# Performance work log

Hardware: AMD Instinct MI355X
Metric: run time of the kernel (lower is better)

The kernel has to match this reference:

```python
import jax, jax.numpy as jnp
import numpy as np

L, H, P = 16384, 1024, 512
DT_MIN, DT_MAX = 1e-3, 1e-1
STEP_RESCALE = 1.0


def setup_inputs() -> dict:
    key = jax.random.key(0)
    ks = jax.random.split(key, 7)
    input_sequence = jax.random.normal(ks[0], (L, H), jnp.float32)
    # eigenvalues with negative real part (left half plane), HiPPO-like imag parts
    Lambda_re = -(jax.random.uniform(ks[1], (P,), jnp.float32) * 0.9 + 0.1)
    Lambda_im = jnp.pi * jnp.arange(P, dtype=jnp.float32)
    B = jax.random.normal(ks[2], (P, H, 2), jnp.float32) / jnp.sqrt(2.0 * H)   # real/imag of B_tilde (P,H)
    C = jax.random.normal(ks[3], (H, P, 2), jnp.float32) / jnp.sqrt(2.0 * P)   # real/imag of C_tilde (H,P)
    D = jax.random.normal(ks[4], (H,), jnp.float32)
    u01 = jax.random.uniform(ks[5], (P, 1), jnp.float32)
    log_step = jnp.log(DT_MIN) + u01 * (jnp.log(DT_MAX) - jnp.log(DT_MIN))     # (P,1)
    return dict(input_sequence=input_sequence, Lambda_re=Lambda_re, Lambda_im=Lambda_im,
                B=B, C=C, D=D, log_step=log_step)


def _binop(q_i, q_j):
    # diagonal linear recurrence composition: (A, b) pairs
    A_i, b_i = q_i
    A_j, b_j = q_j
    return A_j * A_i, A_j * b_i + b_j


def reference(input_sequence, Lambda_re, Lambda_im, B, C, D, log_step):
    Lambda = Lambda_re + 1j * Lambda_im                        # (P,) complex64
    B_tilde = B[..., 0] + 1j * B[..., 1]                       # (P,H)
    C_tilde = C[..., 0] + 1j * C[..., 1]                       # (H,P)
    step = STEP_RESCALE * jnp.exp(log_step[:, 0])              # (P,)
    # ZOH discretization
    Lambda_bar = jnp.exp(Lambda * step)                        # (P,)
    B_bar = ((Lambda_bar - 1.0) / Lambda)[:, None] * B_tilde   # (P,H)
    # Bu_elements: (L,P) complex
    Bu = input_sequence.astype(B_bar.dtype) @ B_bar.T
    Lambda_elems = jnp.broadcast_to(Lambda_bar, Bu.shape)      # (L,P)
    # parallel associative scan over the diagonal recurrence x_t = Lambda_bar*x_{t-1} + Bu_t
    _, xs = jax.lax.associative_scan(_binop, (Lambda_elems, Bu))
    ys = 2.0 * (xs @ C_tilde.T).real                           # conj_sym => factor 2, (L,H)
    return ys + D * input_sequence
```

## Files before the change

kernel.cpp:

```cpp
#include <hip/hip_runtime.h>
#include <math.h>

#define L_SEQ 16384
#define H_DIM 1024
#define P_DIM 512
#define N2P   1024
#define KDIM  1024
#define NKT   16
#define CHUNK 64
#define NCHUNK 256

typedef __attribute__((ext_vector_type(8))) short short8;
typedef __attribute__((ext_vector_type(4))) float f32x4;
typedef __attribute__((address_space(3))) const char* lds3_t;

__device__ __forceinline__ unsigned short f2bf(float f){
    unsigned int u = __float_as_uint(f);
    u = (u + 0x7FFFu + ((u >> 16) & 1u)) >> 16;
    return (unsigned short)u;
}
__device__ __forceinline__ float bf2f(unsigned int lo16){
    return __uint_as_float(lo16 << 16);
}

__global__ void k_prep_lambda(const float* __restrict__ lre, const float* __restrict__ lim,
                              const float* __restrict__ lstep,
                              float* __restrict__ lam, float* __restrict__ coef,
                              float* __restrict__ lpow, float* __restrict__ wtab)
{
    int p = threadIdx.x;
    double step = exp((double)lstep[p]);
    double dr = (double)lre[p], di = (double)lim[p];
    double ar = dr*step, ai = di*step;
    double er = exp(ar);
    double lbr = er*cos(ai), lbi = er*sin(ai);
    lam[2*p] = (float)lbr; lam[2*p+1] = (float)lbi;
    double nr = lbr - 1.0, ni = lbi;
    double d2 = dr*dr + di*di;
    coef[2*p]   = (float)((nr*dr + ni*di)/d2);
    coef[2*p+1] = (float)((ni*dr - nr*di)/d2);
    double pwr = 1.0, pwi = 0.0;
    for (int tt = 63; tt >= 0; --tt){
        wtab[((size_t)tt*P_DIM + p)*2]     = (float)pwr;
        wtab[((size_t)tt*P_DIM + p)*2 + 1] = (float)pwi;
        double t2 = pwr*lbr - pwi*lbi;
        pwi = pwr*lbi + pwi*lbr;
        pwr = t2;
    }
    double xr = lbr, xi = lbi;
    #pragma unroll
    for (int s=0;s<6;s++){ double t = xr*xr - xi*xi; xi = 2.0*xr*xi; xr = t; }
    lpow[2*p] = (float)xr; lpow[2*p+1] = (float)xi;
}

__global__ __launch_bounds__(256)
void k_prep_bc(const float* __restrict__ B, const float* __restrict__ C,
               const float* __restrict__ coef,
               unsigned short* __restrict__ BB, unsigned short* __restrict__ CC)
{
    int bid = blockIdx.x;
    if (bid < 2048){
        int i = bid*256 + threadIdx.x;
        int p = i >> 10, h = i & 1023;
        float br = B[2*i], bi = B[2*i+1];
        float cr = coef[2*p], ci = coef[2*p+1];
        BB[(size_t)(2*p)*H_DIM + h]   = f2bf(cr*br - ci*bi);
        BB[(size_t)(2*p+1)*H_DIM + h] = f2bf(cr*bi + ci*br);
    } else {
        int i = (bid-2048)*256 + threadIdx.x;
        int h = i >> 9, p = i & 511;
        float cr = C[2*i], ci = C[2*i+1];
        CC[(size_t)h*N2P + 2*p]     = f2bf(2.f*cr);
        CC[(size_t)h*N2P + 2*p + 1] = f2bf(-2.f*ci);
    }
}

__global__ __launch_bounds__(256)
void k_cast(const float4* __restrict__ u, unsigned short* __restrict__ o)
{
    int i = blockIdx.x*256 + threadIdx.x;
    float4 a = u[2*i], b = u[2*i+1];
    union { short8 v; unsigned short s[8]; } r;
    r.s[0]=f2bf(a.x); r.s[1]=f2bf(a.y); r.s[2]=f2bf(a.z); r.s[3]=f2bf(a.w);
    r.s[4]=f2bf(b.x); r.s[5]=f2bf(b.y); r.s[6]=f2bf(b.z); r.s[7]=f2bf(b.w);
    *reinterpret_cast<short8*>(o + (size_t)i*8) = r.v;
}

template<int EPI>
__global__ __launch_bounds__(512, 2)
void gemm256(const unsigned short* __restrict__ A, const unsigned short* __restrict__ Bm,
             float* __restrict__ Cf, unsigned short* __restrict__ Cb,
             const float* __restrict__ Dv, const unsigned short* __restrict__ U16,
             const float* __restrict__ wtab, float* __restrict__ aggOut)
{
    __shared__ char lds[131072];
    const int tid  = threadIdx.x;
    const int lane = tid & 63;
    const int wid  = tid >> 6;
    const int wm = wid >> 2, wn = wid & 3;
    const int wg = ((int)blockIdx.x & 7) * 32 + ((int)blockIdx.x >> 3);
    const int tm = wg >> 2, tn = wg & 3;
    const int lr = lane & 15;

    const int scol = ((tid & 7) ^ ((tid >> 3) & 7)) << 3;
    const int srow = tid >> 3;
    const int kc0 = (((lane >> 4)      ^ (lr & 7)) << 4);
    const int kc1 = ((((lane >> 4) | 4) ^ (lr & 7)) << 4);
    const int aSub = wm*16384 + lr*128;
    const int bSub = 32768 + (wn >> 1)*16384 + (wn & 1)*8192 + lr*128;

#define GLOAD(SRC, DST) __builtin_amdgcn_global_load_lds( \
        (const __attribute__((address_space(1))) void*)(SRC), \
        (__attribute__((address_space(3))) void*)(DST), 16, 0, 0)
#define STAGE_A(kt_, h_) do{ \
    char* d_ = lds + (((kt_)&1)<<16) + (h_)*16384 + tid*16; \
    const unsigned short* s_ = A + (size_t)(tm*256 + (h_)*128 + srow)*KDIM + (size_t)(kt_)*64 + scol; \
    GLOAD(s_, d_); GLOAD(s_ + (size_t)64*KDIM, d_ + 8192); }while(0)
#define STAGE_B(kt_, h_) do{ \
    char* d_ = lds + (((kt_)&1)<<16) + 32768 + (h_)*16384 + tid*16; \
    const unsigned short* s_ = Bm + (size_t)(tn*256 + (h_)*128 + srow)*KDIM + (size_t)(kt_)*64 + scol; \
    GLOAD(s_, d_); GLOAD(s_ + (size_t)64*KDIM, d_ + 8192); }while(0)
#define DSR(D, P, IMM) asm volatile("ds_read_b128 %0, %1 offset:" IMM : "=v"(D) : "v"(P))
#define LGKM(N) do{ asm volatile("s_waitcnt lgkmcnt(" #N ")" ::: "memory"); \
                    __builtin_amdgcn_sched_barrier(0); }while(0)
#define VMC4  asm volatile("s_waitcnt vmcnt(4)" ::: "memory")
#define ABAR  asm volatile("s_barrier" ::: "memory")
#define SB0   __builtin_amdgcn_sched_barrier(0)
#define MFMA(a,b,c) __builtin_amdgcn_mfma_f32_16x16x32_bf16(a,b,c,0,0,0)
#define PRIO1 __builtin_amdgcn_s_setprio(1)
#define PRIO0 __builtin_amdgcn_s_setprio(0)

    short8 a1[4], a2[4], bb0[4], bb1[4];
    f32x4 acc[8][4];
    #pragma unroll
    for (int m=0;m<8;m++)
        #pragma unroll
        for (int n=0;n<4;n++) acc[m][n] = (f32x4){0.f,0.f,0.f,0.f};

    STAGE_A(0,0); STAGE_A(0,1); STAGE_B(0,0); STAGE_B(0,1); STAGE_B(1,0); STAGE_B(1,1);
    VMC4; ABAR;

    #pragma unroll 2
    for (int kt = 0; kt < NKT; ++kt) {
        const int sb = (kt & 1) << 16;
        const int tA = (kt+1 < NKT) ? kt+1 : NKT-1;
        const int tB = (kt+2 < NKT) ? kt+2 : NKT-1;
        lds3_t pa0 = (lds3_t)(lds + sb + aSub + kc0);
        lds3_t pa1 = (lds3_t)(lds + sb + aSub + kc1);
        lds3_t pb0 = (lds3_t)(lds + sb + bSub + kc0);
        lds3_t pb1 = (lds3_t)(lds + sb + bSub + kc1);

        DSR(a1[0], pa0, "0");    DSR(a1[1], pa0, "2048");
        DSR(a1[2], pa0, "4096"); DSR(a1[3], pa0, "6144");
        DSR(bb0[0], pb0, "0");    DSR(bb0[1], pb0, "2048");
        DSR(bb0[2], pb0, "4096"); DSR(bb0[3], pb0, "6144");
        STAGE_A(tA, 0); STAGE_A(tA, 1);
        DSR(a2[0], pa0, "8192");  DSR(a2[1], pa0, "10240");
        DSR(a2[2], pa0, "12288"); DSR(a2[3], pa0, "14336");
        LGKM(4);
        PRIO1;
        #pragma unroll
        for (int m=0;m<4;m++)
            #pragma unroll
            for (int n=0;n<4;n++) acc[m][n] = MFMA(a1[m], bb0[n], acc[m][n]);
        PRIO0; SB0;
        DSR(a1[0], pa1, "0");    DSR(a1[1], pa1, "2048");
        DSR(a1[2], pa1, "4096"); DSR(a1[3], pa1, "6144");
        DSR(bb1[0], pb1, "0");    DSR(bb1[1], pb1, "2048");
        DSR(bb1[2], pb1, "4096"); DSR(bb1[3], pb1, "6144");
        LGKM(8);
        PRIO1;
        #pragma unroll
        for (int m=0;m<4;m++)
            #pragma unroll
            for (int n=0;n<4;n++) acc[4+m][n] = MFMA(a2[m], bb0[n], acc[4+m][n]);
        PRIO0; SB0;
        DSR(a2[0], pa1, "8192");  DSR(a2[1], pa1, "10240");
        DSR(a2[2], pa1, "12288"); DSR(a2[3], pa1, "14336");
        LGKM(4);
        ABAR;
        STAGE_B(tB, 0); STAGE_B(tB, 1);
        PRIO1;
        #pragma unroll
        for (int m=0;m<4;m++)
            #pragma unroll
            for (int n=0;n<4;n++) acc[m][n] = MFMA(a1[m], bb1[n], acc[m][n]);
        PRIO0; SB0;
        LGKM(0);
        PRIO1;
        #pragma unroll
        for (int m=0;m<4;m++)
            #pragma unroll
            for (int n=0;n<4;n++) acc[4+m][n] = MFMA(a2[m], bb1[n], acc[4+m][n]);
        PRIO0; SB0;
        VMC4;
        ABAR;
    }
    asm volatile("s_waitcnt vmcnt(0)" ::: "memory");

    if (!EPI){
        const int q = lane >> 4;
        #pragma unroll
        for (int n=0;n<4;n++){
            const int pg = tn*128 + wn*32 + n*8 + (lr >> 1);
            float wr[16], wi[16];
            #pragma unroll
            for (int mm=0;mm<4;mm++)
                #pragma unroll
                for (int j=0;j<4;j++){
                    const float* wp = wtab + ((size_t)(mm*16 + q*4 + j)*P_DIM + pg)*2;
                    wr[mm*4+j] = wp[0]; wi[mm*4+j] = wp[1];
                }
            #pragma unroll
            for (int h=0; h<2; h++){
                float s1 = 0.f, s2 = 0.f;
                #pragma unroll
                for (int mm=0;mm<4;mm++)
                    #pragma unroll
                    for (int j=0;j<4;j++){
                        float x = acc[h*4+mm][n][j];
                        s1 += wr[mm*4+j]*x;
                        s2 += wi[mm*4+j]*x;
                    }
                s1 += __shfl_xor(s1,16); s1 += __shfl_xor(s1,32);
                s2 += __shfl_xor(s2,16); s2 += __shfl_xor(s2,32);
                float s1p = __shfl_xor(s1,1);
                float s2p = __shfl_xor(s2,1);
                if (lane < 16 && !(lr & 1)){
                    int c = 4*tm + 2*wm + h;
                    float* o = aggOut + ((size_t)c*P_DIM + pg)*2;
                    o[0] = s1 - s2p;
                    o[1] = s2 + s1p;
                }
            }
        }
    }

    const int orow0 = tm*256 + wm*128 + (lane>>4)*4;
    const int ocol0 = tn*256 + wn*64 + lr;
    #pragma unroll
    for (int m=0;m<8;m++){
        #pragma unroll
        for (int n=0;n<4;n++){
            int row = orow0 + m*16, col = ocol0 + n*16;
            #pragma unroll
            for (int j=0;j<4;j++){
                size_t idx = (size_t)(row + j)*N2P + col;
                if (EPI) Cf[idx] = acc[m][n][j] + Dv[col]*bf2f(U16[idx]);
                else     Cb[idx] = f2bf(acc[m][n][j]);
            }
        }
    }
#undef GLOAD
#undef STAGE_A
#undef STAGE_B
#undef DSR
#undef LGKM
#undef VMC4
#undef ABAR
#undef SB0
#undef MFMA
#undef PRIO1
#undef PRIO0
}

__global__ __launch_bounds__(256)
void k_scan(float* __restrict__ agg, const float* __restrict__ lpow)
{
    __shared__ float sr[NCHUNK], si[NCHUNK];
    int c = threadIdx.x, p = blockIdx.x;
    float xr = agg[((size_t)c*P_DIM + p)*2];
    float xi = agg[((size_t)c*P_DIM + p)*2 + 1];
    sr[c] = xr; si[c] = xi;
    float wr = lpow[2*p], wi = lpow[2*p+1];
    for (int s=1; s<NCHUNK; s<<=1){
        __syncthreads();
        float ur = 0.f, ui = 0.f;
        if (c >= s){ ur = sr[c-s]; ui = si[c-s]; }
        __syncthreads();
        xr += wr*ur - wi*ui;
        xi += wr*ui + wi*ur;
        sr[c] = xr; si[c] = xi;
        float t = wr*wr - wi*wi; wi = 2.f*wr*wi; wr = t;
    }
    __syncthreads();
    float er = 0.f, ei = 0.f;
    if (c > 0){ er = sr[c-1]; ei = si[c-1]; }
    agg[((size_t)c*P_DIM + p)*2]     = er;
    agg[((size_t)c*P_DIM + p)*2 + 1] = ei;
}

__global__ __launch_bounds__(512)
void k_apply(const unsigned int* __restrict__ Bu, const float* __restrict__ lam,
             const float* __restrict__ xinit, unsigned int* __restrict__ xs)
{
    int p = threadIdx.x, c = blockIdx.x;
    float lrr = lam[2*p], lii = lam[2*p+1];
    float xr = xinit[((size_t)c*P_DIM + p)*2];
    float xi = xinit[((size_t)c*P_DIM + p)*2 + 1];
    const unsigned int* b2 = Bu + (size_t)c*CHUNK*512 + p;
    unsigned int* o = xs + (size_t)c*CHUNK*512 + p;
    #pragma unroll 4
    for (int t=0;t<CHUNK;t++){
        unsigned int b = b2[(size_t)t*512];
        float br = __uint_as_float(b << 16);
        float bi = __uint_as_float(b & 0xffff0000u);
        float tr = lrr*xr - lii*xi + br;
        xi = lrr*xi + lii*xr + bi;
        xr = tr;
        o[(size_t)t*512] = (unsigned int)f2bf(xr) | ((unsigned int)f2bf(xi) << 16);
    }
}

extern "C" void kernel_launch(void* const* d_in, const int* in_sizes, int n_in,
                              void* d_out, int out_size, void* d_ws, size_t ws_size,
                              hipStream_t stream)
{
    const float* u   = (const float*)d_in[0];
    const float* lre = (const float*)d_in[1];
    const float* lim = (const float*)d_in[2];
    const float* B   = (const float*)d_in[3];
    const float* C   = (const float*)d_in[4];
    const float* D   = (const float*)d_in[5];
    const float* ls  = (const float*)d_in[6];
    float* out = (float*)d_out;

    char* w = (char*)d_ws;
    unsigned short* u16  = (unsigned short*)(w + 0);
    unsigned short* xs16 = (unsigned short*)(w + 33554432);
    unsigned short* Bu16 = (unsigned short*)(w + 67108864);
    unsigned short* BB   = (unsigned short*)(w + 100663296);
    unsigned short* CC   = (unsigned short*)(w + 102760448);
    float* lam   = (float*)(w + 104857600);
    float* coef  = (float*)(w + 104861696);
    float* lpow  = (float*)(w + 104865792);
    float* agg   = (float*)(w + 104869888);
    float* wtab  = (float*)(w + 105918464);

    k_prep_lambda<<<1, P_DIM, 0, stream>>>(lre, lim, ls, lam, coef, lpow, wtab);
    k_prep_bc<<<4096, 256, 0, stream>>>(B, C, coef, BB, CC);
    k_cast<<<(L_SEQ*H_DIM)/(256*8), 256, 0, stream>>>((const float4*)u, u16);

    gemm256<0><<<256, 512, 0, stream>>>(u16, BB, nullptr, Bu16, nullptr, nullptr,
                                        wtab, agg);

    k_scan<<<P_DIM, NCHUNK, 0, stream>>>(agg, lpow);
    k_apply<<<NCHUNK, P_DIM, 0, stream>>>((const unsigned int*)Bu16, lam, agg,
                                          (unsigned int*)xs16);

    gemm256<1><<<256, 512, 0, stream>>>(xs16, CC, out, nullptr, D, u16,
                                        nullptr, nullptr);
}
```

Before: 124.9 us.

## Restructure GEMM double-buffer prefetch to one stage ahead and fuse prep kernels

The GEMM prefetch schedule changes from staggered A (one tile ahead) and B (two tiles ahead) loads to a plain double buffer. Both A and B for the next k-tile are now issued into the opposite LDS half during the current iteration, and the mid-iteration barrier before the B staging is removed. Each iteration now ends with a full vmcnt(0) wait, which shortens prefetch depth for B and may expose more global-load latency. Separately, the input bf16 cast kernel is merged into the B/C prep kernel to save one launch.

```diff
diff --git a/kernel.cpp b/kernel.cpp
--- a/kernel.cpp
+++ b/kernel.cpp
@@ -54,9 +54,10 @@
 }
 
 __global__ __launch_bounds__(256)
-void k_prep_bc(const float* __restrict__ B, const float* __restrict__ C,
-               const float* __restrict__ coef,
-               unsigned short* __restrict__ BB, unsigned short* __restrict__ CC)
+void k_prep_misc(const float* __restrict__ B, const float* __restrict__ C,
+                 const float* __restrict__ coef,
+                 unsigned short* __restrict__ BB, unsigned short* __restrict__ CC,
+                 const float4* __restrict__ u, unsigned short* __restrict__ u16)
 {
     int bid = blockIdx.x;
     if (bid < 2048){
@@ -66,24 +67,20 @@
         float cr = coef[2*p], ci = coef[2*p+1];
         BB[(size_t)(2*p)*H_DIM + h]   = f2bf(cr*br - ci*bi);
         BB[(size_t)(2*p+1)*H_DIM + h] = f2bf(cr*bi + ci*br);
-    } else {
+    } else if (bid < 4096){
         int i = (bid-2048)*256 + threadIdx.x;
         int h = i >> 9, p = i & 511;
         float cr = C[2*i], ci = C[2*i+1];
         CC[(size_t)h*N2P + 2*p]     = f2bf(2.f*cr);
         CC[(size_t)h*N2P + 2*p + 1] = f2bf(-2.f*ci);
-    }
-}
-
-__global__ __launch_bounds__(256)
-void k_cast(const float4* __restrict__ u, unsigned short* __restrict__ o)
-{
-    int i = blockIdx.x*256 + threadIdx.x;
-    float4 a = u[2*i], b = u[2*i+1];
-    union { short8 v; unsigned short s[8]; } r;
-    r.s[0]=f2bf(a.x); r.s[1]=f2bf(a.y); r.s[2]=f2bf(a.z); r.s[3]=f2bf(a.w);
-    r.s[4]=f2bf(b.x); r.s[5]=f2bf(b.y); r.s[6]=f2bf(b.z); r.s[7]=f2bf(b.w);
-    *reinterpret_cast<short8*>(o + (size_t)i*8) = r.v;
+    } else {
+        int i = (bid-4096)*256 + threadIdx.x;
+        float4 a = u[2*i], b = u[2*i+1];
+        union { short8 v; unsigned short s[8]; } r;
+        r.s[0]=f2bf(a.x); r.s[1]=f2bf(a.y); r.s[2]=f2bf(a.z); r.s[3]=f2bf(a.w);
+        r.s[4]=f2bf(b.x); r.s[5]=f2bf(b.y); r.s[6]=f2bf(b.z); r.s[7]=f2bf(b.w);
+        *reinterpret_cast<short8*>(u16 + (size_t)i*8) = r.v;
+    }
 }
 
 template<int EPI>
@@ -112,18 +109,18 @@
 #define GLOAD(SRC, DST) __builtin_amdgcn_global_load_lds( \
         (const __attribute__((address_space(1))) void*)(SRC), \
         (__attribute__((address_space(3))) void*)(DST), 16, 0, 0)
-#define STAGE_A(kt_, h_) do{ \
-    char* d_ = lds + (((kt_)&1)<<16) + (h_)*16384 + tid*16; \
-    const unsigned short* s_ = A + (size_t)(tm*256 + (h_)*128 + srow)*KDIM + (size_t)(kt_)*64 + scol; \
+#define STAGE_A(src_, par_, h_) do{ \
+    char* d_ = lds + ((par_)<<16) + (h_)*16384 + tid*16; \
+    const unsigned short* s_ = A + (size_t)(tm*256 + (h_)*128 + srow)*KDIM + (size_t)(src_)*64 + scol; \
     GLOAD(s_, d_); GLOAD(s_ + (size_t)64*KDIM, d_ + 8192); }while(0)
-#define STAGE_B(kt_, h_) do{ \
-    char* d_ = lds + (((kt_)&1)<<16) + 32768 + (h_)*16384 + tid*16; \
-    const unsigned short* s_ = Bm + (size_t)(tn*256 + (h_)*128 + srow)*KDIM + (size_t)(kt_)*64 + scol; \
+#define STAGE_B(src_, par_, h_) do{ \
+    char* d_ = lds + ((par_)<<16) + 32768 + (h_)*16384 + tid*16; \
+    const unsigned short* s_ = Bm + (size_t)(tn*256 + (h_)*128 + srow)*KDIM + (size_t)(src_)*64 + scol; \
     GLOAD(s_, d_); GLOAD(s_ + (size_t)64*KDIM, d_ + 8192); }while(0)
 #define DSR(D, P, IMM) asm volatile("ds_read_b128 %0, %1 offset:" IMM : "=v"(D) : "v"(P))
 #define LGKM(N) do{ asm volatile("s_waitcnt lgkmcnt(" #N ")" ::: "memory"); \
                     __builtin_amdgcn_sched_barrier(0); }while(0)
-#define VMC4  asm volatile("s_waitcnt vmcnt(4)" ::: "memory")
+#define VMC0  asm volatile("s_waitcnt vmcnt(0)" ::: "memory")
 #define ABAR  asm volatile("s_barrier" ::: "memory")
 #define SB0   __builtin_amdgcn_sched_barrier(0)
 #define MFMA(a,b,c) __builtin_amdgcn_mfma_f32_16x16x32_bf16(a,b,c,0,0,0)
@@ -137,14 +134,14 @@
         #pragma unroll
         for (int n=0;n<4;n++) acc[m][n] = (f32x4){0.f,0.f,0.f,0.f};
 
-    STAGE_A(0,0); STAGE_A(0,1); STAGE_B(0,0); STAGE_B(0,1); STAGE_B(1,0); STAGE_B(1,1);
-    VMC4; ABAR;
+    STAGE_A(0,0,0); STAGE_A(0,0,1); STAGE_B(0,0,0); STAGE_B(0,0,1);
+    VMC0; ABAR;
 
     #pragma unroll 2
     for (int kt = 0; kt < NKT; ++kt) {
-        const int sb = (kt & 1) << 16;
-        const int tA = (kt+1 < NKT) ? kt+1 : NKT-1;
-        const int tB = (kt+2 < NKT) ? kt+2 : NKT-1;
+        const int sb   = (kt & 1) << 16;
+        const int dpar = (~kt) & 1;
+        const int src  = (kt+1 < NKT) ? kt+1 : NKT-1;
         lds3_t pa0 = (lds3_t)(lds + sb + aSub + kc0);
         lds3_t pa1 = (lds3_t)(lds + sb + aSub + kc1);
         lds3_t pb0 = (lds3_t)(lds + sb + bSub + kc0);
@@ -154,7 +151,7 @@
         DSR(a1[2], pa0, "4096"); DSR(a1[3], pa0, "6144");
         DSR(bb0[0], pb0, "0");    DSR(bb0[1], pb0, "2048");
         DSR(bb0[2], pb0, "4096"); DSR(bb0[3], pb0, "6144");
-        STAGE_A(tA, 0); STAGE_A(tA, 1);
+        STAGE_A(src, dpar, 0); STAGE_A(src, dpar, 1);
         DSR(a2[0], pa0, "8192");  DSR(a2[1], pa0, "10240");
         DSR(a2[2], pa0, "12288"); DSR(a2[3], pa0, "14336");
         LGKM(4);
@@ -168,6 +165,7 @@
         DSR(a1[2], pa1, "4096"); DSR(a1[3], pa1, "6144");
         DSR(bb1[0], pb1, "0");    DSR(bb1[1], pb1, "2048");
         DSR(bb1[2], pb1, "4096"); DSR(bb1[3], pb1, "6144");
+        STAGE_B(src, dpar, 0); STAGE_B(src, dpar, 1);
         LGKM(8);
         PRIO1;
         #pragma unroll
@@ -178,8 +176,6 @@
         DSR(a2[0], pa1, "8192");  DSR(a2[1], pa1, "10240");
         DSR(a2[2], pa1, "12288"); DSR(a2[3], pa1, "14336");
         LGKM(4);
-        ABAR;
-        STAGE_B(tB, 0); STAGE_B(tB, 1);
         PRIO1;
         #pragma unroll
         for (int m=0;m<4;m++)
@@ -193,10 +189,9 @@
             #pragma unroll
             for (int n=0;n<4;n++) acc[4+m][n] = MFMA(a2[m], bb1[n], acc[4+m][n]);
         PRIO0; SB0;
-        VMC4;
+        VMC0;
         ABAR;
     }
-    asm volatile("s_waitcnt vmcnt(0)" ::: "memory");
 
     if (!EPI){
         const int q = lane >> 4;
@@ -256,7 +251,7 @@
 #undef STAGE_B
 #undef DSR
 #undef LGKM
-#undef VMC4
+#undef VMC0
 #undef ABAR
 #undef SB0
 #undef MFMA
@@ -338,8 +333,7 @@
     float* wtab  = (float*)(w + 105918464);
 
     k_prep_lambda<<<1, P_DIM, 0, stream>>>(lre, lim, ls, lam, coef, lpow, wtab);
-    k_prep_bc<<<4096, 256, 0, stream>>>(B, C, coef, BB, CC);
-    k_cast<<<(L_SEQ*H_DIM)/(256*8), 256, 0, stream>>>((const float4*)u, u16);
+    k_prep_misc<<<12288, 256, 0, stream>>>(B, C, coef, BB, CC, (const float4*)u, u16);
 
     gemm256<0><<<256, 512, 0, stream>>>(u16, BB, nullptr, Bu16, nullptr, nullptr,
                                         wtab, agg);
```

New measurement: 123.1 us. Within noise of the previous version (-1.4%).
